# Kernel tuning notes

Measured on AMD Instinct MI355X. Metric: run time of the kernel, lower is better.

Reference implementation:

```python
import jax, jax.numpy as jnp
import numpy as np

K = 7          # window kernel size
PAD = 3        # padding so out spatial == in spatial (stride=1, dilation=1)
BN_EPS = 1e-5


def conv1x1(x, w, b):
    # x: (b,c,h,w), w: (o,c), b: (o,)
    return jnp.einsum('bchw,oc->bohw', x, w) + b[None, :, None, None]


def bn_relu(x, bn):
    # bn: (4, C) rows = gamma, beta, running_mean, running_var (inference-mode BN)
    g, bta, m, v = bn[0], bn[1], bn[2], bn[3]
    scale = g / jnp.sqrt(v + BN_EPS)
    y = (x - m[None, :, None, None]) * scale[None, :, None, None] + bta[None, :, None, None]
    return jax.nn.relu(y)


def extract_patches(x):
    # Equivalent of F.unfold(x, K, padding=PAD, stride=1) reshaped to (b, C, K*K, H, W).
    # Ordering matches torch: channel major, kernel positions row-major.
    b, c, h, w = x.shape
    xp = jnp.pad(x, ((0, 0), (0, 0), (PAD, PAD), (PAD, PAD)))
    ps = [xp[:, :, i:i + h, j:j + w] for i in range(K) for j in range(K)]
    return jnp.stack(ps, axis=2)  # (b, c, K*K, h, w)


def setup_inputs() -> dict:
    key = jax.random.key(0)
    ks = jax.random.split(key, 20)
    Cin, Ck, Cv, Co = 256, 64, 128, 256
    b, h, w = 2, 96, 96

    def wgt(k, o, c):
        return jax.random.normal(k, (o, c), jnp.float32) * 0.05

    def bias(k, o):
        return jax.random.normal(k, (o,), jnp.float32) * 0.02

    def bn(k, c):
        g = 1.0 + 0.1 * jax.random.normal(k, (c,), jnp.float32)
        bta = 0.1 * jax.random.normal(jax.random.fold_in(k, 1), (c,), jnp.float32)
        m = 0.05 * jax.random.normal(jax.random.fold_in(k, 2), (c,), jnp.float32)
        v = 1.0 + 0.1 * jax.random.uniform(jax.random.fold_in(k, 3), (c,), jnp.float32)
        return jnp.stack([g, bta, m, v])  # (4, c)

    return {
        'x': jax.random.normal(ks[0], (b, Cin, h, w), jnp.float32),
        'fk_w1': wgt(ks[1], Ck, Cin), 'fk_b1': bias(ks[2], Ck), 'fk_bn1': bn(ks[3], Ck),
        'fk_w2': wgt(ks[4], Ck, Ck), 'fk_b2': bias(ks[5], Ck), 'fk_bn2': bn(ks[6], Ck),
        'fq_w1': wgt(ks[7], Ck, Cin), 'fq_b1': bias(ks[8], Ck), 'fq_bn1': bn(ks[9], Ck),
        'fq_w2': wgt(ks[10], Ck, Ck), 'fq_b2': bias(ks[11], Ck), 'fq_bn2': bn(ks[12], Ck),
        'fv_w': wgt(ks[13], Cv, Cin), 'fv_b': bias(ks[14], Cv),
        'W_w': wgt(ks[15], Co, Cv), 'W_b': bias(ks[16], Co),
    }


def reference(x, fk_w1, fk_b1, fk_bn1, fk_w2, fk_b2, fk_bn2,
              fq_w1, fq_b1, fq_bn1, fq_w2, fq_b2, fq_bn2,
              fv_w, fv_b, W_w, W_b):
    # scale=1 -> no pooling. stride=1, dilation=1, pad=3, k=7 -> out spatial == in spatial.
    value = conv1x1(x, fv_w, fv_b)                       # (b, Cv, H, W)
    unfold_value = extract_patches(value)                # (b, Cv, 49, H, W)

    k1 = bn_relu(conv1x1(x, fk_w1, fk_b1), fk_bn1)
    key = bn_relu(conv1x1(k1, fk_w2, fk_b2), fk_bn2)     # (b, Ck, H, W)
    unfold_key = extract_patches(key)                    # (b, Ck, 49, H, W)

    q1 = bn_relu(conv1x1(x, fq_w1, fq_b1), fq_bn1)
    query = bn_relu(conv1x1(q1, fq_w2, fq_b2), fq_bn2)   # (b, Ck, H, W)
    # start_index = dilation*(k//2) - padding = 0; stride=1 -> query slice is identity.

    sim = jnp.sum(unfold_key * query[:, :, None], axis=1, keepdims=True)  # (b,1,49,H,W)
    sim = jax.nn.softmax(sim, axis=2)
    context = jnp.sum(sim * unfold_value, axis=2)        # (b, Cv, H, W)
    context = conv1x1(context, W_w, W_b)                 # (b, Co, H, W)
    # F.interpolate to (h, w) with align_corners=True is identity (same size).
    return context
```

## Files before the change

### kernel.cpp

```cpp
#include <hip/hip_runtime.h>
#include <hip/hip_bf16.h>

typedef _Float16 f16;
typedef _Float16 f16x4 __attribute__((ext_vector_type(4)));
typedef _Float16 f16x8 __attribute__((ext_vector_type(8)));
typedef float f32x4 __attribute__((ext_vector_type(4)));

#define HH 96
#define WW 96
#define HWs 9216
#define BN_EPS 1e-5f

#define OFF_ACT1 0u
#define OFF_ACT2 4718592u

__global__ __launch_bounds__(256) void conv12(
    const float* __restrict__ x,
    const float* __restrict__ fv_w, const float* __restrict__ fk_w1, const float* __restrict__ fq_w1,
    const float* __restrict__ fk_w2, const float* __restrict__ fq_w2,
    const float* __restrict__ fv_b,
    const float* __restrict__ fk_b1, const float* __restrict__ fk_bn1,
    const float* __restrict__ fq_b1, const float* __restrict__ fq_bn1,
    const float* __restrict__ fk_b2, const float* __restrict__ fk_bn2,
    const float* __restrict__ fq_b2, const float* __restrict__ fq_bn2,
    f16* __restrict__ act1, f16* __restrict__ act2)
{
  __shared__ f16 As[32 * 264];
  __shared__ f16 Bs[2][256 * 40];
  __shared__ f16 kqs[2][32 * 72];
  const int tid = threadIdx.x;
  const int l = tid & 63, w = tid >> 6;
  const int bb = blockIdx.y;
  const int p0 = blockIdx.x * 32;
  const int lrow = l & 15, lk = (l >> 4) * 8;

  const int spx = tid & 31, scg = tid >> 5;
#pragma unroll
  for (int it = 0; it < 8; ++it) {
    int ch = it * 32 + scg * 4;
    f16x4 av;
#pragma unroll
    for (int j = 0; j < 4; j++)
      av[j] = (f16)x[((size_t)bb * 256 + ch + j) * HWs + p0 + spx];
    *(f16x4*)&As[spx * 264 + ch] = av;
  }

  auto stageW = [&](int ks, int bf) {
#pragma unroll
    for (int it = 0; it < 4; it++) {
      int tt = it * 256 + tid;
      int row = tt >> 2, seg = tt & 3;
      const float* srcp;
      if (it < 2)       srcp = fv_w  + (size_t)row * 256;
      else if (it == 2) srcp = fk_w1 + (size_t)(row - 128) * 256;
      else              srcp = fq_w1 + (size_t)(row - 192) * 256;
      float4 u0 = *(const float4*)&srcp[ks * 32 + seg * 8];
      float4 u1 = *(const float4*)&srcp[ks * 32 + seg * 8 + 4];
      f16x8 h = {(f16)u0.x, (f16)u0.y, (f16)u0.z, (f16)u0.w,
                 (f16)u1.x, (f16)u1.y, (f16)u1.z, (f16)u1.w};
      *(f16x8*)&Bs[bf][row * 40 + seg * 8] = h;
    }
  };

  f32x4 acc[2][4];
#pragma unroll
  for (int i = 0; i < 2; i++)
#pragma unroll
    for (int j = 0; j < 4; j++) acc[i][j] = (f32x4){0.f, 0.f, 0.f, 0.f};

  stageW(0, 0);
#pragma unroll 1
  for (int ks = 0; ks < 8; ks++) {
    __syncthreads();
    if (ks < 7) stageW(ks + 1, (ks + 1) & 1);
    f16x8 a[2], b[4];
#pragma unroll
    for (int mi = 0; mi < 2; mi++)
      a[mi] = *(const f16x8*)&As[(mi * 16 + lrow) * 264 + ks * 32 + lk];
#pragma unroll
    for (int nj = 0; nj < 4; nj++)
      b[nj] = *(const f16x8*)&Bs[ks & 1][(w * 64 + nj * 16 + lrow) * 40 + lk];
#pragma unroll
    for (int mi = 0; mi < 2; mi++)
#pragma unroll
      for (int nj = 0; nj < 4; nj++)
        acc[mi][nj] = __builtin_amdgcn_mfma_f32_16x16x32_f16(a[mi], b[nj], acc[mi][nj], 0, 0, 0);
  }

#pragma unroll
  for (int nj = 0; nj < 4; nj++) {
    int cout = w * 64 + nj * 16 + lrow;
    float s, t;
    if (w < 2) { s = 1.0f; t = fv_b[cout]; }
    else {
      int j = nj * 16 + lrow;
      const float* bn = (w == 2) ? fk_bn1 : fq_bn1;
      const float* bs = (w == 2) ? fk_b1 : fq_b1;
      float g = bn[j], be = bn[64 + j], m = bn[128 + j], v = bn[192 + j];
      s = g * rsqrtf(v + BN_EPS); t = (bs[j] - m) * s + be;
    }
#pragma unroll
    for (int mi = 0; mi < 2; mi++)
#pragma unroll
      for (int r = 0; r < 4; r++) {
        int px = mi * 16 + (l >> 4) * 4 + r;
        float v = acc[mi][nj][r] * s + t;
        if (w < 2) {
          act1[((size_t)bb * HWs + p0 + px) * 128 + cout] = (f16)v;
        } else {
          kqs[w - 2][px * 72 + (nj * 16 + lrow)] = (f16)fmaxf(v, 0.f);
        }
      }
  }
  __syncthreads();

  const int sel = w >> 1, half = w & 1;
  const float* W2s = sel ? fq_w2 : fk_w2;
  f32x4 acc2[2][2];
#pragma unroll
  for (int i = 0; i < 2; i++)
#pragma unroll
    for (int j = 0; j < 2; j++) acc2[i][j] = (f32x4){0.f, 0.f, 0.f, 0.f};
#pragma unroll
  for (int ks = 0; ks < 2; ks++) {
    f16x8 a2[2], b2[2];
#pragma unroll
    for (int mi = 0; mi < 2; mi++)
      a2[mi] = *(const f16x8*)&kqs[sel][(mi * 16 + lrow) * 72 + ks * 32 + lk];
#pragma unroll
    for (int nj = 0; nj < 2; nj++) {
      const float* wp = &W2s[(size_t)(half * 32 + nj * 16 + lrow) * 64 + ks * 32 + lk];
      float4 u0 = *(const float4*)&wp[0];
      float4 u1 = *(const float4*)&wp[4];
      b2[nj] = (f16x8){(f16)u0.x, (f16)u0.y, (f16)u0.z, (f16)u0.w,
                       (f16)u1.x, (f16)u1.y, (f16)u1.z, (f16)u1.w};
    }
#pragma unroll
    for (int mi = 0; mi < 2; mi++)
#pragma unroll
      for (int nj = 0; nj < 2; nj++)
        acc2[mi][nj] = __builtin_amdgcn_mfma_f32_16x16x32_f16(a2[mi], b2[nj], acc2[mi][nj], 0, 0, 0);
  }
#pragma unroll
  for (int nj = 0; nj < 2; nj++) {
    int j2 = half * 32 + nj * 16 + lrow;
    int c2 = sel * 64 + j2;
    const float* bn = sel ? fq_bn2 : fk_bn2;
    const float* bs = sel ? fq_b2 : fk_b2;
    float g = bn[j2], be = bn[64 + j2], m = bn[128 + j2], v = bn[192 + j2];
    float s = g * rsqrtf(v + BN_EPS), t = (bs[j2] - m) * s + be;
#pragma unroll
    for (int mi = 0; mi < 2; mi++)
#pragma unroll
      for (int r = 0; r < 4; r++) {
        int px = mi * 16 + (l >> 4) * 4 + r;
        float vv = fmaxf(acc2[mi][nj][r] * s + t, 0.f);
        act2[((size_t)bb * HWs + p0 + px) * 128 + c2] = (f16)vv;
      }
  }
}

__global__ __launch_bounds__(256) void attn_final(const f16* __restrict__ act1,
                                                  const f16* __restrict__ act2,
                                                  const float* __restrict__ W_w,
                                                  const float* __restrict__ W_b,
                                                  float* __restrict__ out)
{
  __shared__ float Ps[64 * 52];
  __shared__ f16 buf[208 * 136];
  const int tid = threadIdx.x;
  const int l = tid & 63, w = tid >> 6;
  const int bb = blockIdx.z;
  const int x0 = blockIdx.x * 8, y0 = blockIdx.y * 8;
  const f16* a2 = act2 + (size_t)bb * HWs * 128;
  const f16* a1 = act1 + (size_t)bb * HWs * 128;
  f16* Qs = buf;
  f16* Ks = buf + 64 * 72;
  const int lrow = l & 15, lk = (l >> 4) * 8;

#pragma unroll
  for (int it = 0; it < 2; it++) {
    int t = it * 256 + tid;
    int q = t >> 3, seg = t & 7;
    int gp = (y0 + (q >> 3)) * WW + x0 + (q & 7);
    *(f16x8*)&Qs[q * 72 + seg * 8] = *(const f16x8*)&a2[(size_t)gp * 128 + 64 + seg * 8];
  }
  for (int t = tid; t < 1664; t += 256) {
    int kk = t >> 3, seg = t & 7;
    int ky = (kk * 4682) >> 16, kx = kk - 14 * ky;
    int gy = y0 - 3 + ky, gx = x0 - 3 + kx;
    f16x8 v = {(f16)0, (f16)0, (f16)0, (f16)0, (f16)0, (f16)0, (f16)0, (f16)0};
    if (kk < 196 && (unsigned)gy < (unsigned)HH && (unsigned)gx < (unsigned)WW)
      v = *(const f16x8*)&a2[((size_t)(gy * WW + gx)) * 128 + seg * 8];
    *(f16x8*)&Ks[kk * 72 + seg * 8] = v;
  }
  f16x8 vv[13];
  const int vk0 = tid >> 4, vseg = tid & 15;
#pragma unroll
  for (int it = 0; it < 13; ++it) {
    int kk = vk0 + it * 16;
    int ky = (kk * 4682) >> 16, kx = kk - 14 * ky;
    int gy = y0 - 3 + ky, gx = x0 - 3 + kx;
    f16x8 v = {(f16)0, (f16)0, (f16)0, (f16)0, (f16)0, (f16)0, (f16)0, (f16)0};
    if (kk < 196 && (unsigned)gy < (unsigned)HH && (unsigned)gx < (unsigned)WW)
      v = *(const f16x8*)&a1[((size_t)(gy * WW + gx)) * 128 + vseg * 8];
    vv[it] = v;
  }
  __syncthreads();

  f32x4 sc[13];
#pragma unroll
  for (int nj = 0; nj < 13; nj++) sc[nj] = (f32x4){0.f, 0.f, 0.f, 0.f};
#pragma unroll
  for (int ks = 0; ks < 2; ks++) {
    f16x8 aq = *(const f16x8*)&Qs[(w * 16 + lrow) * 72 + ks * 32 + lk];
#pragma unroll
    for (int nj = 0; nj < 13; nj++) {
      f16x8 bk = *(const f16x8*)&Ks[(nj * 16 + lrow) * 72 + ks * 32 + lk];
      sc[nj] = __builtin_amdgcn_mfma_f32_16x16x32_f16(aq, bk, sc[nj], 0, 0, 0);
    }
  }
  const int r0 = w * 16 + (l >> 4) * 4;
#pragma unroll
  for (int nj = 0; nj < 13; nj++) {
    int c = nj * 16 + lrow;
    int ky = (c * 4682) >> 16, kx = c - 14 * ky;
#pragma unroll
    for (int r = 0; r < 4; r++) {
      int qy = (r0 + r) >> 3, qx = (r0 + r) & 7;
      bool valid = ((unsigned)(ky - qy) < 7u) && ((unsigned)(kx - qx) < 7u);
      if (!valid) sc[nj][r] = -1e30f;
    }
  }
  float mx[4], sm[4], inv[4];
#pragma unroll
  for (int r = 0; r < 4; r++) {
    mx[r] = -1e30f;
#pragma unroll
    for (int nj = 0; nj < 13; nj++) mx[r] = fmaxf(mx[r], sc[nj][r]);
  }
#pragma unroll
  for (int off = 1; off < 16; off <<= 1)
#pragma unroll
    for (int r = 0; r < 4; r++) mx[r] = fmaxf(mx[r], __shfl_xor(mx[r], off));
#pragma unroll
  for (int r = 0; r < 4; r++) sm[r] = 0.f;
#pragma unroll
  for (int nj = 0; nj < 13; nj++)
#pragma unroll
    for (int r = 0; r < 4; r++) {
      float e = __expf(sc[nj][r] - mx[r]);
      sc[nj][r] = e; sm[r] += e;
    }
#pragma unroll
  for (int off = 1; off < 16; off <<= 1)
#pragma unroll
    for (int r = 0; r < 4; r++) sm[r] += __shfl_xor(sm[r], off);
#pragma unroll
  for (int r = 0; r < 4; r++) inv[r] = 1.0f / sm[r];
#pragma unroll
  for (int nj = 0; nj < 13; nj++) {
    int c = nj * 16 + lrow;
    int ky = (c * 4682) >> 16, kx = c - 14 * ky;
#pragma unroll
    for (int r = 0; r < 4; r++) {
      int qy = (r0 + r) >> 3, qx = (r0 + r) & 7;
      int dy = ky - qy, dx = kx - qx;
      if (((unsigned)dy < 7u) && ((unsigned)dx < 7u))
        Ps[(r0 + r) * 52 + dy * 7 + dx] = sc[nj][r] * inv[r];
    }
  }
  __syncthreads();

  f16* Vs = buf;
#pragma unroll
  for (int it = 0; it < 13; ++it)
    *(f16x8*)&Vs[(size_t)(vk0 + it * 16) * 136 + vseg * 8] = vv[it];
  __syncthreads();

  const int q = tid >> 2;
  const int qy = q >> 3, qx = q & 7;
  const int ch0 = (tid & 3) * 32;
  float acc[32];
#pragma unroll
  for (int i = 0; i < 32; i++) acc[i] = 0.f;
#pragma unroll
  for (int dy = 0; dy < 7; dy++)
#pragma unroll
    for (int dx = 0; dx < 7; dx++) {
      float p = Ps[q * 52 + dy * 7 + dx];
      int kk = (qy + dy) * 14 + qx + dx;
      const f16* vp = &Vs[kk * 136 + ch0];
#pragma unroll
      for (int s = 0; s < 4; s++) {
        f16x8 v = *(const f16x8*)&vp[s * 8];
#pragma unroll
        for (int j = 0; j < 8; j++) acc[s * 8 + j] += (float)v[j] * p;
      }
    }
  __syncthreads();

  f16* ctxs = buf;
#pragma unroll
  for (int s = 0; s < 4; s++) {
    f16x8 o;
#pragma unroll
    for (int j = 0; j < 8; j++) o[j] = (f16)acc[s * 8 + j];
    *(f16x8*)&ctxs[q * 136 + ch0 + s * 8] = o;
  }
  __syncthreads();

  f32x4 fac[4][4];
#pragma unroll
  for (int i = 0; i < 4; i++)
#pragma unroll
    for (int j = 0; j < 4; j++) fac[i][j] = (f32x4){0.f, 0.f, 0.f, 0.f};
#pragma unroll
  for (int ks = 0; ks < 4; ks++) {
    f16x8 a3[4], b3[4];
#pragma unroll
    for (int mi = 0; mi < 4; mi++) {
      const float* wp = &W_w[(size_t)(w * 64 + mi * 16 + lrow) * 128 + ks * 32 + lk];
      float4 u0 = *(const float4*)&wp[0];
      float4 u1 = *(const float4*)&wp[4];
      a3[mi] = (f16x8){(f16)u0.x, (f16)u0.y, (f16)u0.z, (f16)u0.w,
                       (f16)u1.x, (f16)u1.y, (f16)u1.z, (f16)u1.w};
    }
#pragma unroll
    for (int nj = 0; nj < 4; nj++)
      b3[nj] = *(const f16x8*)&ctxs[(nj * 16 + lrow) * 136 + ks * 32 + lk];
#pragma unroll
    for (int mi = 0; mi < 4; mi++)
#pragma unroll
      for (int nj = 0; nj < 4; nj++)
        fac[mi][nj] = __builtin_amdgcn_mfma_f32_16x16x32_f16(a3[mi], b3[nj], fac[mi][nj], 0, 0, 0);
  }
#pragma unroll
  for (int mi = 0; mi < 4; mi++)
#pragma unroll
    for (int r = 0; r < 4; r++) {
      int cout = w * 64 + mi * 16 + (l >> 4) * 4 + r;
      float bias = W_b[cout];
#pragma unroll
      for (int nj = 0; nj < 4; nj++) {
        int px = nj * 16 + lrow;
        int gp = (y0 + (px >> 3)) * WW + x0 + (px & 7);
        out[((size_t)bb * 256 + cout) * HWs + gp] = fac[mi][nj][r] + bias;
      }
    }
}

extern "C" void kernel_launch(void* const* d_in, const int* in_sizes, int n_in,
                              void* d_out, int out_size, void* d_ws, size_t ws_size,
                              hipStream_t stream) {
  (void)in_sizes; (void)n_in; (void)out_size; (void)ws_size;
  const float* x      = (const float*)d_in[0];
  const float* fk_w1  = (const float*)d_in[1];
  const float* fk_b1  = (const float*)d_in[2];
  const float* fk_bn1 = (const float*)d_in[3];
  const float* fk_w2  = (const float*)d_in[4];
  const float* fk_b2  = (const float*)d_in[5];
  const float* fk_bn2 = (const float*)d_in[6];
  const float* fq_w1  = (const float*)d_in[7];
  const float* fq_b1  = (const float*)d_in[8];
  const float* fq_bn1 = (const float*)d_in[9];
  const float* fq_w2  = (const float*)d_in[10];
  const float* fq_b2  = (const float*)d_in[11];
  const float* fq_bn2 = (const float*)d_in[12];
  const float* fv_w   = (const float*)d_in[13];
  const float* fv_b   = (const float*)d_in[14];
  const float* W_w    = (const float*)d_in[15];
  const float* W_b    = (const float*)d_in[16];
  char* wsb = (char*)d_ws;
  float* out = (float*)d_out;

  f16* act1 = (f16*)(wsb + OFF_ACT1);
  f16* act2 = (f16*)(wsb + OFF_ACT2);

  conv12<<<dim3(288, 2), dim3(256), 0, stream>>>(
      x, fv_w, fk_w1, fq_w1, fk_w2, fq_w2,
      fv_b, fk_b1, fk_bn1, fq_b1, fq_bn1,
      fk_b2, fk_bn2, fq_b2, fq_bn2, act1, act2);

  attn_final<<<dim3(12, 12, 2), dim3(256), 0, stream>>>(act1, act2, W_w, W_b, out);
}
```

Measured before the change: 164.0 us.

## Split value window into two channel halves with overlapped prefetch in attention kernel

The attention kernel now loads the first 64 value channels into shared memory alongside Q and K. The second half is prefetched into registers while the first-half weighted sum runs, then written over the Q/K region for a second pass. This trims the K/V tile loads to exactly 196 window rows and packs shared memory to about 78 KB. The aim is to cut register pressure from the old 13-register value buffer, hide value-load latency behind compute and drop one barrier. The cost is an extra pass over the softmax weights and more complex shared-memory aliasing.

```diff
diff --git a/kernel.cpp b/kernel.cpp
--- a/kernel.cpp
+++ b/kernel.cpp
@@ -166,16 +166,20 @@
                                                   const float* __restrict__ W_b,
                                                   float* __restrict__ out)
 {
-  __shared__ float Ps[64 * 52];
-  __shared__ f16 buf[208 * 136];
+  __shared__ __align__(16) char smem[78208];
+  f16* Qs   = (f16*)smem;
+  f16* Ks   = (f16*)(smem + 9216);
+  f16* Vs0  = (f16*)(smem + 37440);
+  f16* Vs1  = (f16*)smem;
+  f16* ctxs = (f16*)(smem + 37440);
+  float* Ps = (float*)(smem + 65664);
+
   const int tid = threadIdx.x;
   const int l = tid & 63, w = tid >> 6;
   const int bb = blockIdx.z;
   const int x0 = blockIdx.x * 8, y0 = blockIdx.y * 8;
   const f16* a2 = act2 + (size_t)bb * HWs * 128;
   const f16* a1 = act1 + (size_t)bb * HWs * 128;
-  f16* Qs = buf;
-  f16* Ks = buf + 64 * 72;
   const int lrow = l & 15, lk = (l >> 4) * 8;
 
 #pragma unroll
@@ -185,26 +189,23 @@
     int gp = (y0 + (q >> 3)) * WW + x0 + (q & 7);
     *(f16x8*)&Qs[q * 72 + seg * 8] = *(const f16x8*)&a2[(size_t)gp * 128 + 64 + seg * 8];
   }
-  for (int t = tid; t < 1664; t += 256) {
+  for (int t = tid; t < 1568; t += 256) {
     int kk = t >> 3, seg = t & 7;
     int ky = (kk * 4682) >> 16, kx = kk - 14 * ky;
     int gy = y0 - 3 + ky, gx = x0 - 3 + kx;
     f16x8 v = {(f16)0, (f16)0, (f16)0, (f16)0, (f16)0, (f16)0, (f16)0, (f16)0};
-    if (kk < 196 && (unsigned)gy < (unsigned)HH && (unsigned)gx < (unsigned)WW)
+    if ((unsigned)gy < (unsigned)HH && (unsigned)gx < (unsigned)WW)
       v = *(const f16x8*)&a2[((size_t)(gy * WW + gx)) * 128 + seg * 8];
     *(f16x8*)&Ks[kk * 72 + seg * 8] = v;
   }
-  f16x8 vv[13];
-  const int vk0 = tid >> 4, vseg = tid & 15;
-#pragma unroll
-  for (int it = 0; it < 13; ++it) {
-    int kk = vk0 + it * 16;
+  for (int t = tid; t < 1568; t += 256) {
+    int kk = t >> 3, seg = t & 7;
     int ky = (kk * 4682) >> 16, kx = kk - 14 * ky;
     int gy = y0 - 3 + ky, gx = x0 - 3 + kx;
     f16x8 v = {(f16)0, (f16)0, (f16)0, (f16)0, (f16)0, (f16)0, (f16)0, (f16)0};
-    if (kk < 196 && (unsigned)gy < (unsigned)HH && (unsigned)gx < (unsigned)WW)
-      v = *(const f16x8*)&a1[((size_t)(gy * WW + gx)) * 128 + vseg * 8];
-    vv[it] = v;
+    if ((unsigned)gy < (unsigned)HH && (unsigned)gx < (unsigned)WW)
+      v = *(const f16x8*)&a1[((size_t)(gy * WW + gx)) * 128 + seg * 8];
+    *(f16x8*)&Vs0[kk * 72 + seg * 8] = v;
   }
   __syncthreads();
 
@@ -228,7 +229,7 @@
 #pragma unroll
     for (int r = 0; r < 4; r++) {
       int qy = (r0 + r) >> 3, qx = (r0 + r) & 7;
-      bool valid = ((unsigned)(ky - qy) < 7u) && ((unsigned)(kx - qx) < 7u);
+      bool valid = (c < 196) && ((unsigned)(ky - qy) < 7u) && ((unsigned)(kx - qx) < 7u);
       if (!valid) sc[nj][r] = -1e30f;
     }
   }
@@ -266,47 +267,85 @@
     for (int r = 0; r < 4; r++) {
       int qy = (r0 + r) >> 3, qx = (r0 + r) & 7;
       int dy = ky - qy, dx = kx - qx;
-      if (((unsigned)dy < 7u) && ((unsigned)dx < 7u))
-        Ps[(r0 + r) * 52 + dy * 7 + dx] = sc[nj][r] * inv[r];
-    }
-  }
-  __syncthreads();
-
-  f16* Vs = buf;
-#pragma unroll
-  for (int it = 0; it < 13; ++it)
-    *(f16x8*)&Vs[(size_t)(vk0 + it * 16) * 136 + vseg * 8] = vv[it];
+      if (c < 196 && ((unsigned)dy < 7u) && ((unsigned)dx < 7u))
+        Ps[(r0 + r) * 49 + dy * 7 + dx] = sc[nj][r] * inv[r];
+    }
+  }
   __syncthreads();
 
   const int q = tid >> 2;
   const int qy = q >> 3, qx = q & 7;
-  const int ch0 = (tid & 3) * 32;
-  float acc[32];
-#pragma unroll
-  for (int i = 0; i < 32; i++) acc[i] = 0.f;
+  const int ch0 = (tid & 3) * 16;
+
+  f16x8 vreg[7];
+#pragma unroll
+  for (int it = 0; it < 7; ++it) {
+    int idx = it * 256 + tid;
+    f16x8 v = {(f16)0, (f16)0, (f16)0, (f16)0, (f16)0, (f16)0, (f16)0, (f16)0};
+    if (idx < 1568) {
+      int kk = idx >> 3, seg = idx & 7;
+      int ky = (kk * 4682) >> 16, kx = kk - 14 * ky;
+      int gy = y0 - 3 + ky, gx = x0 - 3 + kx;
+      if ((unsigned)gy < (unsigned)HH && (unsigned)gx < (unsigned)WW)
+        v = *(const f16x8*)&a1[((size_t)(gy * WW + gx)) * 128 + 64 + seg * 8];
+    }
+    vreg[it] = v;
+  }
+
+  float acc0[16], acc1[16];
+#pragma unroll
+  for (int i = 0; i < 16; i++) acc0[i] = 0.f;
 #pragma unroll
   for (int dy = 0; dy < 7; dy++)
 #pragma unroll
     for (int dx = 0; dx < 7; dx++) {
-      float p = Ps[q * 52 + dy * 7 + dx];
+      float p = Ps[q * 49 + dy * 7 + dx];
       int kk = (qy + dy) * 14 + qx + dx;
-      const f16* vp = &Vs[kk * 136 + ch0];
-#pragma unroll
-      for (int s = 0; s < 4; s++) {
-        f16x8 v = *(const f16x8*)&vp[s * 8];
-#pragma unroll
-        for (int j = 0; j < 8; j++) acc[s * 8 + j] += (float)v[j] * p;
+      const f16* vp = &Vs0[kk * 72 + ch0];
+      f16x8 v0 = *(const f16x8*)&vp[0];
+      f16x8 v1 = *(const f16x8*)&vp[8];
+#pragma unroll
+      for (int j = 0; j < 8; j++) {
+        acc0[j] += (float)v0[j] * p;
+        acc0[8 + j] += (float)v1[j] * p;
       }
     }
+#pragma unroll
+  for (int it = 0; it < 7; ++it) {
+    int idx = it * 256 + tid;
+    if (idx < 1568)
+      *(f16x8*)&Vs1[(idx >> 3) * 72 + (idx & 7) * 8] = vreg[it];
+  }
   __syncthreads();
 
-  f16* ctxs = buf;
-#pragma unroll
-  for (int s = 0; s < 4; s++) {
-    f16x8 o;
-#pragma unroll
-    for (int j = 0; j < 8; j++) o[j] = (f16)acc[s * 8 + j];
-    *(f16x8*)&ctxs[q * 136 + ch0 + s * 8] = o;
+#pragma unroll
+  for (int i = 0; i < 16; i++) acc1[i] = 0.f;
+#pragma unroll
+  for (int dy = 0; dy < 7; dy++)
+#pragma unroll
+    for (int dx = 0; dx < 7; dx++) {
+      float p = Ps[q * 49 + dy * 7 + dx];
+      int kk = (qy + dy) * 14 + qx + dx;
+      const f16* vp = &Vs1[kk * 72 + ch0];
+      f16x8 v0 = *(const f16x8*)&vp[0];
+      f16x8 v1 = *(const f16x8*)&vp[8];
+#pragma unroll
+      for (int j = 0; j < 8; j++) {
+        acc1[j] += (float)v0[j] * p;
+        acc1[8 + j] += (float)v1[j] * p;
+      }
+    }
+  {
+    f16x8 o0, o1, o2, o3;
+#pragma unroll
+    for (int j = 0; j < 8; j++) {
+      o0[j] = (f16)acc0[j];     o1[j] = (f16)acc0[8 + j];
+      o2[j] = (f16)acc1[j];     o3[j] = (f16)acc1[8 + j];
+    }
+    *(f16x8*)&ctxs[q * 136 + ch0]          = o0;
+    *(f16x8*)&ctxs[q * 136 + ch0 + 8]      = o1;
+    *(f16x8*)&ctxs[q * 136 + 64 + ch0]     = o2;
+    *(f16x8*)&ctxs[q * 136 + 64 + ch0 + 8] = o3;
   }
   __syncthreads();
 
```

After: 179.7 us. +9.6%, slower.
